# Optimization experiments

Measured on AMD Instinct MI355X. Metric: run time of the kernel, lower is better.

## Reference

```python
import jax, jax.numpy as jnp
import numpy as np

N = 262144          # num keyframes
E = 1048576         # num visual links (edges)
DT = 0.1            # IMU integration step
L1, L2, L3, L4 = 1.0, 0.5, 2.0, 0.5
EPS = 1e-6

# ---- quaternion helpers (pypose convention: q = [x, y, z, w]) ----

def qmul(q1, q2):
    v1, w1 = q1[..., :3], q1[..., 3:4]
    v2, w2 = q2[..., :3], q2[..., 3:4]
    w = w1 * w2 - jnp.sum(v1 * v2, axis=-1, keepdims=True)
    v = w1 * v2 + w2 * v1 + jnp.cross(v1, v2)
    return jnp.concatenate([v, w], axis=-1)

def qconj(q):
    return jnp.concatenate([-q[..., :3], q[..., 3:4]], axis=-1)

def qrot(q, x):
    # rotate vector x by unit quaternion q: x + 2*cross(v, cross(v,x) + w*x)
    v, w = q[..., :3], q[..., 3:4]
    return x + 2.0 * jnp.cross(v, jnp.cross(v, x) + w * x)

def so3_log(q):
    # log map of unit quaternion -> axis-angle phi (..., 3)
    v, w = q[..., :3], q[..., 3:4]
    n = jnp.linalg.norm(v, axis=-1, keepdims=True)
    n_safe = jnp.where(n < EPS, 1.0, n)
    theta = 2.0 * jnp.arctan2(n, w)
    w_safe = jnp.where(jnp.abs(w) < EPS, 1.0, w)
    factor = jnp.where(n < EPS, 2.0 / w_safe, theta / n_safe)
    return factor * v

def se3_inv(p):
    t, q = p[..., :3], p[..., 3:]
    qi = qconj(q)
    ti = -qrot(qi, t)
    return jnp.concatenate([ti, qi], axis=-1)

def se3_mul(p1, p2):
    t1, q1 = p1[..., :3], p1[..., 3:]
    t2, q2 = p2[..., :3], p2[..., 3:]
    t = t1 + qrot(q1, t2)
    return jnp.concatenate([t, qmul(q1, q2)], axis=-1)

def se3_log(p):
    # returns se(3) tensor [tau, phi] (pypose order) with tau = Jl^{-1}(phi) t
    t, q = p[..., :3], p[..., 3:]
    phi = so3_log(q)
    th = jnp.linalg.norm(phi, axis=-1, keepdims=True)
    th_safe = jnp.where(th < EPS, 1.0, th)
    coef = jnp.where(
        th < EPS,
        1.0 / 12.0 + th * th / 720.0,
        1.0 / (th_safe * th_safe)
        - (1.0 + jnp.cos(th_safe)) / (2.0 * th_safe * jnp.sin(th_safe)),
    )
    pxt = jnp.cross(phi, t)
    tau = t - 0.5 * pxt + coef * jnp.cross(phi, pxt)
    return jnp.concatenate([tau, phi], axis=-1)


def setup_inputs() -> dict:
    key = jax.random.key(0)
    ks = jax.random.split(key, 8)

    def unit_quat(k, n):
        q = jax.random.normal(k, (n, 4), dtype=jnp.float32)
        return q / jnp.linalg.norm(q, axis=-1, keepdims=True)

    pose = jnp.concatenate(
        [jax.random.normal(ks[0], (N, 3), dtype=jnp.float32),
         unit_quat(ks[1], N)], axis=-1)
    vel = jax.random.normal(ks[2], (N, 3), dtype=jnp.float32)
    vmot = jnp.concatenate(
        [0.1 * jax.random.normal(ks[3], (E, 3), dtype=jnp.float32),
         unit_quat(ks[4], E)], axis=-1)
    imu_drot = unit_quat(ks[5], N - 1)
    body_dvel = 0.1 * jax.random.normal(ks[6], (N - 1, 3), dtype=jnp.float32)
    body_dpos = 0.1 * jax.random.normal(ks[7], (N - 1, 3), dtype=jnp.float32)
    vlink = jax.random.randint(jax.random.fold_in(key, 99), (E, 2), 0, N)
    return dict(pose=pose, vel=vel, vmot=vmot, imu_drot=imu_drot,
                body_dvel=body_dvel, body_dpos=body_dpos, vlink=vlink)


def reference(pose, vel, vmot, imu_drot, body_dvel, body_dpos, vlink):
    trans, rot = pose[:, :3], pose[:, 3:]
    r1 = rot[:-1]

    # IMU model: world-frame increments (rotation-dependent, as in original)
    imu_dvel = qrot(r1, body_dvel)                      # world_dvel(pose.rotation())
    imu_dpos = qrot(r1, body_dpos) + vel[:-1] * DT      # world_dpos(rot, vel)

    # pose-graph residual: Log(vmot^{-1} @ pose1^{-1} @ pose2)  [E, 6]
    pose1 = pose[vlink[:, 0]]
    pose2 = pose[vlink[:, 1]]
    err = se3_mul(se3_inv(vmot), se3_mul(se3_inv(pose1), pose2))
    pgerr = se3_log(err)

    # adjacent velocity residual [N-1, 3]
    adjvelerr = imu_dvel - jnp.diff(vel, axis=0)

    # IMU rotation residual: Log(imu_drot @ R1^{-1} @ R2)  [N-1, 3]
    q_rel = qmul(imu_drot, qmul(qconj(rot[:-1]), rot[1:]))
    imuroterr = so3_log(q_rel)

    # translation/velocity residual [N-1, 3]
    transvelerr = imu_dpos - jnp.diff(trans, axis=0)

    return jnp.concatenate([
        L1 * pgerr.reshape(-1),
        L2 * adjvelerr.reshape(-1),
        L3 * imuroterr.reshape(-1),
        L4 * transvelerr.reshape(-1),
    ], axis=0)
```

## Files before the change

### kernel.cpp

```cpp
#include <hip/hip_runtime.h>
#include <math.h>

constexpr int   NN  = 262144;
constexpr int   NE  = 1048576;
constexpr float DTc = 0.1f;
constexpr float W1 = 1.0f, W2 = 0.5f, W3 = 2.0f, W4 = 0.5f;
constexpr float EPSc = 1e-6f;

typedef float    __attribute__((ext_vector_type(2))) f32x2;
typedef float    __attribute__((ext_vector_type(4))) f32x4;
typedef float    __attribute__((ext_vector_type(4), aligned(4))) f32x4u;
typedef float    __attribute__((ext_vector_type(2), aligned(4))) f32x2u;
typedef int      __attribute__((ext_vector_type(2))) i32x2;
typedef _Float16 __attribute__((ext_vector_type(8))) f16x8;

struct V3 { float x, y, z; };
struct Q4 { float x, y, z, w; };

__device__ __forceinline__ V3 v3(float x, float y, float z) { V3 r{x, y, z}; return r; }
__device__ __forceinline__ V3 vadd(V3 a, V3 b) { return v3(a.x + b.x, a.y + b.y, a.z + b.z); }
__device__ __forceinline__ V3 vsub(V3 a, V3 b) { return v3(a.x - b.x, a.y - b.y, a.z - b.z); }
__device__ __forceinline__ V3 vscale(float s, V3 a) { return v3(s * a.x, s * a.y, s * a.z); }
__device__ __forceinline__ V3 vcross(V3 a, V3 b) {
    return v3(a.y * b.z - a.z * b.y, a.z * b.x - a.x * b.z, a.x * b.y - a.y * b.x);
}
__device__ __forceinline__ float vdot(V3 a, V3 b) { return a.x * b.x + a.y * b.y + a.z * b.z; }

__device__ __forceinline__ Q4 qmul(Q4 a, Q4 b) {
    Q4 r;
    r.w = a.w * b.w - (a.x * b.x + a.y * b.y + a.z * b.z);
    r.x = a.w * b.x + b.w * a.x + (a.y * b.z - a.z * b.y);
    r.y = a.w * b.y + b.w * a.y + (a.z * b.x - a.x * b.z);
    r.z = a.w * b.z + b.w * a.z + (a.x * b.y - a.y * b.x);
    return r;
}
__device__ __forceinline__ Q4 qconj(Q4 q) { Q4 r{-q.x, -q.y, -q.z, q.w}; return r; }
__device__ __forceinline__ V3 qrot(Q4 q, V3 x) {
    V3 v = v3(q.x, q.y, q.z);
    V3 c1 = vadd(vcross(v, x), vscale(q.w, x));
    return vadd(x, vscale(2.0f, vcross(v, c1)));
}
__device__ __forceinline__ V3 so3_log(Q4 q) {
    V3 v = v3(q.x, q.y, q.z);
    float n = sqrtf(vdot(v, v));
    float theta = 2.0f * atan2f(n, q.w);
    float factor;
    if (n < EPSc) {
        float w_safe = (fabsf(q.w) < EPSc) ? 1.0f : q.w;
        factor = 2.0f / w_safe;
    } else {
        factor = theta / n;
    }
    return vscale(factor, v);
}

struct TP { V3 tau; V3 phi; };

__device__ __forceinline__ TP edge_residual(V3 tm, Q4 qm, V3 t1, Q4 q1,
                                            V3 t2, Q4 q2) {
    Q4 qa = qconj(q1);
    V3 tb = qrot(qa, vsub(t2, t1));
    Q4 qb = qmul(qa, q2);
    Q4 qc = qconj(qm);
    V3 te = qrot(qc, vsub(tb, tm));
    Q4 qe = qmul(qc, qb);

    V3 phi = so3_log(qe);
    float th = sqrtf(vdot(phi, phi));
    float coef;
    if (th < EPSc) {
        coef = 1.0f / 12.0f + th * th / 720.0f;
    } else {
        float s, c;
        sincosf(th, &s, &c);
        coef = 1.0f / (th * th) - (1.0f + c) / (2.0f * th * s);
    }
    V3 pxt = vcross(phi, te);
    V3 tau = vadd(vsub(te, vscale(0.5f, pxt)), vscale(coef, vcross(phi, pxt)));
    TP r; r.tau = tau; r.phi = phi; return r;
}

__global__ __launch_bounds__(256) void node_pack_kernel(
    const float* __restrict__ pose, const float* __restrict__ vel,
    const float* __restrict__ imu_drot, const float* __restrict__ body_dvel,
    const float* __restrict__ body_dpos, f16x8* __restrict__ ppH,
    float* __restrict__ out)
{
    int i = blockIdx.x * blockDim.x + threadIdx.x;
    if (i >= NN) return;
    f32x4u pa0 = *(const f32x4u*)(pose + 7 * (size_t)i);
    f32x4u pa1 = *(const f32x4u*)(pose + 7 * (size_t)i + 3);
    f16x8 rec = {(_Float16)pa0.x, (_Float16)pa0.y, (_Float16)pa0.z,
                 (_Float16)pa1.x, (_Float16)pa1.y, (_Float16)pa1.z,
                 (_Float16)pa1.w, (_Float16)0.0f};
    ppH[i] = rec;
    if (i >= NN - 1) return;

    V3 tr1 = v3(pa0.x, pa0.y, pa0.z); Q4 r1 = {pa1.x, pa1.y, pa1.z, pa1.w};
    f32x4u pb0 = *(const f32x4u*)(pose + 7 * (size_t)(i + 1));
    f32x4u pb1 = *(const f32x4u*)(pose + 7 * (size_t)(i + 1) + 3);
    V3 tr2 = v3(pb0.x, pb0.y, pb0.z); Q4 r2 = {pb1.x, pb1.y, pb1.z, pb1.w};

    f32x4u vv = __builtin_nontemporal_load((const f32x4u*)(vel + 3 * (size_t)i));
    f32x2u vw = __builtin_nontemporal_load((const f32x2u*)(vel + 3 * (size_t)i + 4));
    V3 v1 = v3(vv.x, vv.y, vv.z);
    V3 v2 = v3(vv.w, vw.x, vw.y);
    f32x2u bv0 = __builtin_nontemporal_load((const f32x2u*)(body_dvel + 3 * (size_t)i));
    float  bv2 = __builtin_nontemporal_load(body_dvel + 3 * (size_t)i + 2);
    f32x2u bp0 = __builtin_nontemporal_load((const f32x2u*)(body_dpos + 3 * (size_t)i));
    float  bp2 = __builtin_nontemporal_load(body_dpos + 3 * (size_t)i + 2);
    V3 bdv = v3(bv0.x, bv0.y, bv2);
    V3 bdp = v3(bp0.x, bp0.y, bp2);
    f32x4 id4 = __builtin_nontemporal_load((const f32x4*)(imu_drot + 4 * (size_t)i));
    Q4 idr = {id4.x, id4.y, id4.z, id4.w};

    V3 imu_dvel = qrot(r1, bdv);
    V3 adjvel = vsub(imu_dvel, vsub(v2, v1));
    Q4 qrel = qmul(idr, qmul(qconj(r1), r2));
    V3 imurot = so3_log(qrel);
    V3 imu_dpos = vadd(qrot(r1, bdp), vscale(DTc, v1));
    V3 transvel = vsub(imu_dpos, vsub(tr2, tr1));

    size_t base = (size_t)6 * NE;
    size_t nm1 = (size_t)(NN - 1);
    float* oa = out + base + 3 * (size_t)i;
    __builtin_nontemporal_store(W2 * adjvel.x, oa);
    __builtin_nontemporal_store(W2 * adjvel.y, oa + 1);
    __builtin_nontemporal_store(W2 * adjvel.z, oa + 2);
    float* ob = out + base + 3 * nm1 + 3 * (size_t)i;
    __builtin_nontemporal_store(W3 * imurot.x, ob);
    __builtin_nontemporal_store(W3 * imurot.y, ob + 1);
    __builtin_nontemporal_store(W3 * imurot.z, ob + 2);
    float* oc = out + base + 6 * nm1 + 3 * (size_t)i;
    __builtin_nontemporal_store(W4 * transvel.x, oc);
    __builtin_nontemporal_store(W4 * transvel.y, oc + 1);
    __builtin_nontemporal_store(W4 * transvel.z, oc + 2);
}

__global__ __launch_bounds__(256) void edge_kernel(
    const float* __restrict__ vmot, const int* __restrict__ vlink,
    const f16x8* __restrict__ ppH, float* __restrict__ out)
{
    __shared__ float smv[256 * 7];
    int e0 = blockIdx.x * 256;
    const f32x4* src = (const f32x4*)(vmot + (size_t)e0 * 7);
    {
        int idx = threadIdx.x;
        ((f32x4*)smv)[idx] = __builtin_nontemporal_load(src + idx);
        idx += 256;
        if (idx < 448) ((f32x4*)smv)[idx] = __builtin_nontemporal_load(src + idx);
    }
    int e = e0 + threadIdx.x;
    i32x2 l = __builtin_nontemporal_load((const i32x2*)vlink + e);
    f16x8 g1 = ppH[l.x];
    f16x8 g2 = ppH[l.y];
    __syncthreads();
    float m[7];
#pragma unroll
    for (int k = 0; k < 7; ++k) m[k] = smv[7 * threadIdx.x + k];

    TP r = edge_residual(
        v3(m[0], m[1], m[2]), Q4{m[3], m[4], m[5], m[6]},
        v3((float)g1[0], (float)g1[1], (float)g1[2]),
        Q4{(float)g1[3], (float)g1[4], (float)g1[5], (float)g1[6]},
        v3((float)g2[0], (float)g2[1], (float)g2[2]),
        Q4{(float)g2[3], (float)g2[4], (float)g2[5], (float)g2[6]});

    f32x2* o2 = (f32x2*)(out + 6 * (size_t)e);
    f32x2 a = {W1 * r.tau.x, W1 * r.tau.y};
    f32x2 b = {W1 * r.tau.z, W1 * r.phi.x};
    f32x2 c = {W1 * r.phi.y, W1 * r.phi.z};
    __builtin_nontemporal_store(a, o2);
    __builtin_nontemporal_store(b, o2 + 1);
    __builtin_nontemporal_store(c, o2 + 2);
}

__global__ __launch_bounds__(256) void vigraph_fallback(
    const float* __restrict__ pose, const float* __restrict__ vel,
    const float* __restrict__ vmot, const float* __restrict__ imu_drot,
    const float* __restrict__ body_dvel, const float* __restrict__ body_dpos,
    const int* __restrict__ vlink, float* __restrict__ out)
{
    int tid = blockIdx.x * blockDim.x + threadIdx.x;
    if (tid < NE) {
        int e = tid;
        const float* pm = vmot + 7 * (size_t)e;
        int i1 = vlink[2 * (size_t)e];
        int i2 = vlink[2 * (size_t)e + 1];
        const float* p1 = pose + 7 * (size_t)i1;
        const float* p2 = pose + 7 * (size_t)i2;
        TP r = edge_residual(v3(pm[0], pm[1], pm[2]), Q4{pm[3], pm[4], pm[5], pm[6]},
                             v3(p1[0], p1[1], p1[2]), Q4{p1[3], p1[4], p1[5], p1[6]},
                             v3(p2[0], p2[1], p2[2]), Q4{p2[3], p2[4], p2[5], p2[6]});
        float* o = out + 6 * (size_t)e;
        o[0] = W1 * r.tau.x; o[1] = W1 * r.tau.y; o[2] = W1 * r.tau.z;
        o[3] = W1 * r.phi.x; o[4] = W1 * r.phi.y; o[5] = W1 * r.phi.z;
    } else {
        int i = tid - NE;
        if (i >= NN - 1) return;
        const float* pa = pose + 7 * (size_t)i;
        const float* pb = pose + 7 * (size_t)(i + 1);
        V3 tr1 = v3(pa[0], pa[1], pa[2]); Q4 r1 = {pa[3], pa[4], pa[5], pa[6]};
        V3 tr2 = v3(pb[0], pb[1], pb[2]); Q4 r2 = {pb[3], pb[4], pb[5], pb[6]};
        V3 v1 = v3(vel[3 * (size_t)i], vel[3 * (size_t)i + 1], vel[3 * (size_t)i + 2]);
        V3 v2 = v3(vel[3 * (size_t)(i + 1)], vel[3 * (size_t)(i + 1) + 1], vel[3 * (size_t)(i + 1) + 2]);
        V3 bdv = v3(body_dvel[3 * (size_t)i], body_dvel[3 * (size_t)i + 1], body_dvel[3 * (size_t)i + 2]);
        V3 bdp = v3(body_dpos[3 * (size_t)i], body_dpos[3 * (size_t)i + 1], body_dpos[3 * (size_t)i + 2]);
        Q4 idr = {imu_drot[4 * (size_t)i], imu_drot[4 * (size_t)i + 1],
                  imu_drot[4 * (size_t)i + 2], imu_drot[4 * (size_t)i + 3]};
        V3 imu_dvel = qrot(r1, bdv);
        V3 adjvel = vsub(imu_dvel, vsub(v2, v1));
        Q4 qrel = qmul(idr, qmul(qconj(r1), r2));
        V3 imurot = so3_log(qrel);
        V3 imu_dpos = vadd(qrot(r1, bdp), vscale(DTc, v1));
        V3 transvel = vsub(imu_dpos, vsub(tr2, tr1));
        size_t base = (size_t)6 * NE;
        size_t nm1 = (size_t)(NN - 1);
        float* oa = out + base + 3 * (size_t)i;
        oa[0] = W2 * adjvel.x; oa[1] = W2 * adjvel.y; oa[2] = W2 * adjvel.z;
        float* ob = out + base + 3 * nm1 + 3 * (size_t)i;
        ob[0] = W3 * imurot.x; ob[1] = W3 * imurot.y; ob[2] = W3 * imurot.z;
        float* oc = out + base + 6 * nm1 + 3 * (size_t)i;
        oc[0] = W4 * transvel.x; oc[1] = W4 * transvel.y; oc[2] = W4 * transvel.z;
    }
}

extern "C" void kernel_launch(void* const* d_in, const int* in_sizes, int n_in,
                              void* d_out, int out_size, void* d_ws, size_t ws_size,
                              hipStream_t stream) {
    const float* pose      = (const float*)d_in[0];
    const float* vel       = (const float*)d_in[1];
    const float* vmot      = (const float*)d_in[2];
    const float* imu_drot  = (const float*)d_in[3];
    const float* body_dvel = (const float*)d_in[4];
    const float* body_dpos = (const float*)d_in[5];
    const int*   vlink     = (const int*)d_in[6];
    float* out = (float*)d_out;

    const size_t table_bytes = (size_t)NN * 16;
    if (ws_size >= table_bytes) {
        f16x8* ppH = (f16x8*)d_ws;
        node_pack_kernel<<<NN / 256, 256, 0, stream>>>(pose, vel, imu_drot,
                                                       body_dvel, body_dpos, ppH, out);
        edge_kernel<<<NE / 256, 256, 0, stream>>>(vmot, vlink, ppH, out);
    } else {
        int total = NE + (NN - 1);
        int grid = (total + 255) / 256;
        vigraph_fallback<<<grid, 256, 0, stream>>>(pose, vel, vmot, imu_drot,
                                                   body_dvel, body_dpos, vlink, out);
    }
}
```

Baseline: 39.71 us.

## Split pose packing from node residuals and interleave node work into edge kernel

The node kernel is reduced to a minimal fp16 pose-pack pass, and the IMU/node residual work moves into the edge kernel. Blocks are interleaved four edge blocks to one node block, so the bandwidth-heavy node residual work overlaps with the gather-bound edge work. The edge path also drops the shared-memory staging of vmot and its __syncthreads in favour of direct unaligned vector loads per thread. The trade-offs are uncoalesced per-thread vmot loads and a second read of pose in the fused kernel.

```diff
diff --git a/kernel.cpp b/kernel.cpp
--- a/kernel.cpp
+++ b/kernel.cpp
@@ -6,6 +6,10 @@
 constexpr float DTc = 0.1f;
 constexpr float W1 = 1.0f, W2 = 0.5f, W3 = 2.0f, W4 = 0.5f;
 constexpr float EPSc = 1e-6f;
+
+constexpr int NB_EDGE = NE / 256;
+constexpr int NB_NODE = NN / 256;
+constexpr int NB_TOT  = NB_EDGE + NB_NODE;
 
 typedef float    __attribute__((ext_vector_type(2))) f32x2;
 typedef float    __attribute__((ext_vector_type(4))) f32x4;
@@ -80,99 +84,96 @@
     TP r; r.tau = tau; r.phi = phi; return r;
 }
 
-__global__ __launch_bounds__(256) void node_pack_kernel(
+__global__ __launch_bounds__(256) void pack_kernel(const float* __restrict__ pose,
+                                                   f16x8* __restrict__ ppH) {
+    int i = blockIdx.x * blockDim.x + threadIdx.x;
+    if (i >= NN) return;
+    f32x4u a = *(const f32x4u*)(pose + 7 * (size_t)i);
+    f32x4u b = *(const f32x4u*)(pose + 7 * (size_t)i + 3);
+    f16x8 rec = {(_Float16)a.x, (_Float16)a.y, (_Float16)a.z,
+                 (_Float16)b.x, (_Float16)b.y, (_Float16)b.z,
+                 (_Float16)b.w, (_Float16)0.0f};
+    ppH[i] = rec;
+}
+
+__global__ __launch_bounds__(256) void fused_kernel(
     const float* __restrict__ pose, const float* __restrict__ vel,
-    const float* __restrict__ imu_drot, const float* __restrict__ body_dvel,
-    const float* __restrict__ body_dpos, f16x8* __restrict__ ppH,
+    const float* __restrict__ vmot, const float* __restrict__ imu_drot,
+    const float* __restrict__ body_dvel, const float* __restrict__ body_dpos,
+    const int* __restrict__ vlink, const f16x8* __restrict__ ppH,
     float* __restrict__ out)
 {
-    int i = blockIdx.x * blockDim.x + threadIdx.x;
-    if (i >= NN) return;
-    f32x4u pa0 = *(const f32x4u*)(pose + 7 * (size_t)i);
-    f32x4u pa1 = *(const f32x4u*)(pose + 7 * (size_t)i + 3);
-    f16x8 rec = {(_Float16)pa0.x, (_Float16)pa0.y, (_Float16)pa0.z,
-                 (_Float16)pa1.x, (_Float16)pa1.y, (_Float16)pa1.z,
-                 (_Float16)pa1.w, (_Float16)0.0f};
-    ppH[i] = rec;
-    if (i >= NN - 1) return;
-
-    V3 tr1 = v3(pa0.x, pa0.y, pa0.z); Q4 r1 = {pa1.x, pa1.y, pa1.z, pa1.w};
-    f32x4u pb0 = *(const f32x4u*)(pose + 7 * (size_t)(i + 1));
-    f32x4u pb1 = *(const f32x4u*)(pose + 7 * (size_t)(i + 1) + 3);
-    V3 tr2 = v3(pb0.x, pb0.y, pb0.z); Q4 r2 = {pb1.x, pb1.y, pb1.z, pb1.w};
-
-    f32x4u vv = __builtin_nontemporal_load((const f32x4u*)(vel + 3 * (size_t)i));
-    f32x2u vw = __builtin_nontemporal_load((const f32x2u*)(vel + 3 * (size_t)i + 4));
-    V3 v1 = v3(vv.x, vv.y, vv.z);
-    V3 v2 = v3(vv.w, vw.x, vw.y);
-    f32x2u bv0 = __builtin_nontemporal_load((const f32x2u*)(body_dvel + 3 * (size_t)i));
-    float  bv2 = __builtin_nontemporal_load(body_dvel + 3 * (size_t)i + 2);
-    f32x2u bp0 = __builtin_nontemporal_load((const f32x2u*)(body_dpos + 3 * (size_t)i));
-    float  bp2 = __builtin_nontemporal_load(body_dpos + 3 * (size_t)i + 2);
-    V3 bdv = v3(bv0.x, bv0.y, bv2);
-    V3 bdp = v3(bp0.x, bp0.y, bp2);
-    f32x4 id4 = __builtin_nontemporal_load((const f32x4*)(imu_drot + 4 * (size_t)i));
-    Q4 idr = {id4.x, id4.y, id4.z, id4.w};
-
-    V3 imu_dvel = qrot(r1, bdv);
-    V3 adjvel = vsub(imu_dvel, vsub(v2, v1));
-    Q4 qrel = qmul(idr, qmul(qconj(r1), r2));
-    V3 imurot = so3_log(qrel);
-    V3 imu_dpos = vadd(qrot(r1, bdp), vscale(DTc, v1));
-    V3 transvel = vsub(imu_dpos, vsub(tr2, tr1));
-
-    size_t base = (size_t)6 * NE;
-    size_t nm1 = (size_t)(NN - 1);
-    float* oa = out + base + 3 * (size_t)i;
-    __builtin_nontemporal_store(W2 * adjvel.x, oa);
-    __builtin_nontemporal_store(W2 * adjvel.y, oa + 1);
-    __builtin_nontemporal_store(W2 * adjvel.z, oa + 2);
-    float* ob = out + base + 3 * nm1 + 3 * (size_t)i;
-    __builtin_nontemporal_store(W3 * imurot.x, ob);
-    __builtin_nontemporal_store(W3 * imurot.y, ob + 1);
-    __builtin_nontemporal_store(W3 * imurot.z, ob + 2);
-    float* oc = out + base + 6 * nm1 + 3 * (size_t)i;
-    __builtin_nontemporal_store(W4 * transvel.x, oc);
-    __builtin_nontemporal_store(W4 * transvel.y, oc + 1);
-    __builtin_nontemporal_store(W4 * transvel.z, oc + 2);
-}
-
-__global__ __launch_bounds__(256) void edge_kernel(
-    const float* __restrict__ vmot, const int* __restrict__ vlink,
-    const f16x8* __restrict__ ppH, float* __restrict__ out)
-{
-    __shared__ float smv[256 * 7];
-    int e0 = blockIdx.x * 256;
-    const f32x4* src = (const f32x4*)(vmot + (size_t)e0 * 7);
-    {
-        int idx = threadIdx.x;
-        ((f32x4*)smv)[idx] = __builtin_nontemporal_load(src + idx);
-        idx += 256;
-        if (idx < 448) ((f32x4*)smv)[idx] = __builtin_nontemporal_load(src + idx);
-    }
-    int e = e0 + threadIdx.x;
-    i32x2 l = __builtin_nontemporal_load((const i32x2*)vlink + e);
-    f16x8 g1 = ppH[l.x];
-    f16x8 g2 = ppH[l.y];
-    __syncthreads();
-    float m[7];
-#pragma unroll
-    for (int k = 0; k < 7; ++k) m[k] = smv[7 * threadIdx.x + k];
-
-    TP r = edge_residual(
-        v3(m[0], m[1], m[2]), Q4{m[3], m[4], m[5], m[6]},
-        v3((float)g1[0], (float)g1[1], (float)g1[2]),
-        Q4{(float)g1[3], (float)g1[4], (float)g1[5], (float)g1[6]},
-        v3((float)g2[0], (float)g2[1], (float)g2[2]),
-        Q4{(float)g2[3], (float)g2[4], (float)g2[5], (float)g2[6]});
-
-    f32x2* o2 = (f32x2*)(out + 6 * (size_t)e);
-    f32x2 a = {W1 * r.tau.x, W1 * r.tau.y};
-    f32x2 b = {W1 * r.tau.z, W1 * r.phi.x};
-    f32x2 c = {W1 * r.phi.y, W1 * r.phi.z};
-    __builtin_nontemporal_store(a, o2);
-    __builtin_nontemporal_store(b, o2 + 1);
-    __builtin_nontemporal_store(c, o2 + 2);
+    int b = blockIdx.x;
+    int g = b / 5, rdx = b - 5 * g;
+    if (rdx < 4) {
+        int eb = g * 4 + rdx;
+        int e  = eb * 256 + threadIdx.x;
+        i32x2 l = __builtin_nontemporal_load((const i32x2*)vlink + e);
+        const float* pm = vmot + 7 * (size_t)e;
+        f32x4u ma = __builtin_nontemporal_load((const f32x4u*)(pm));
+        f32x4u mb = __builtin_nontemporal_load((const f32x4u*)(pm + 3));
+        f16x8 g1 = ppH[l.x];
+        f16x8 g2 = ppH[l.y];
+
+        TP r = edge_residual(
+            v3(ma.x, ma.y, ma.z), Q4{mb.x, mb.y, mb.z, mb.w},
+            v3((float)g1[0], (float)g1[1], (float)g1[2]),
+            Q4{(float)g1[3], (float)g1[4], (float)g1[5], (float)g1[6]},
+            v3((float)g2[0], (float)g2[1], (float)g2[2]),
+            Q4{(float)g2[3], (float)g2[4], (float)g2[5], (float)g2[6]});
+
+        f32x2* o2 = (f32x2*)(out + 6 * (size_t)e);
+        f32x2 a = {W1 * r.tau.x, W1 * r.tau.y};
+        f32x2 bb = {W1 * r.tau.z, W1 * r.phi.x};
+        f32x2 c = {W1 * r.phi.y, W1 * r.phi.z};
+        __builtin_nontemporal_store(a, o2);
+        __builtin_nontemporal_store(bb, o2 + 1);
+        __builtin_nontemporal_store(c, o2 + 2);
+    } else {
+        int i = g * 256 + threadIdx.x;
+        if (i >= NN - 1) return;
+        f32x4u pa0 = __builtin_nontemporal_load((const f32x4u*)(pose + 7 * (size_t)i));
+        f32x4u pa1 = __builtin_nontemporal_load((const f32x4u*)(pose + 7 * (size_t)i + 3));
+        V3 tr1 = v3(pa0.x, pa0.y, pa0.z); Q4 r1 = {pa1.x, pa1.y, pa1.z, pa1.w};
+        f32x4u pb0 = __builtin_nontemporal_load((const f32x4u*)(pose + 7 * (size_t)(i + 1)));
+        f32x4u pb1 = __builtin_nontemporal_load((const f32x4u*)(pose + 7 * (size_t)(i + 1) + 3));
+        V3 tr2 = v3(pb0.x, pb0.y, pb0.z); Q4 r2 = {pb1.x, pb1.y, pb1.z, pb1.w};
+
+        f32x4u vv = __builtin_nontemporal_load((const f32x4u*)(vel + 3 * (size_t)i));
+        f32x2u vw = __builtin_nontemporal_load((const f32x2u*)(vel + 3 * (size_t)i + 4));
+        V3 v1 = v3(vv.x, vv.y, vv.z);
+        V3 v2 = v3(vv.w, vw.x, vw.y);
+        f32x2u bv0 = __builtin_nontemporal_load((const f32x2u*)(body_dvel + 3 * (size_t)i));
+        float  bv2 = __builtin_nontemporal_load(body_dvel + 3 * (size_t)i + 2);
+        f32x2u bp0 = __builtin_nontemporal_load((const f32x2u*)(body_dpos + 3 * (size_t)i));
+        float  bp2 = __builtin_nontemporal_load(body_dpos + 3 * (size_t)i + 2);
+        V3 bdv = v3(bv0.x, bv0.y, bv2);
+        V3 bdp = v3(bp0.x, bp0.y, bp2);
+        f32x4 id4 = __builtin_nontemporal_load((const f32x4*)(imu_drot + 4 * (size_t)i));
+        Q4 idr = {id4.x, id4.y, id4.z, id4.w};
+
+        V3 imu_dvel = qrot(r1, bdv);
+        V3 adjvel = vsub(imu_dvel, vsub(v2, v1));
+        Q4 qrel = qmul(idr, qmul(qconj(r1), r2));
+        V3 imurot = so3_log(qrel);
+        V3 imu_dpos = vadd(qrot(r1, bdp), vscale(DTc, v1));
+        V3 transvel = vsub(imu_dpos, vsub(tr2, tr1));
+
+        size_t base = (size_t)6 * NE;
+        size_t nm1 = (size_t)(NN - 1);
+        float* oa = out + base + 3 * (size_t)i;
+        __builtin_nontemporal_store(W2 * adjvel.x, oa);
+        __builtin_nontemporal_store(W2 * adjvel.y, oa + 1);
+        __builtin_nontemporal_store(W2 * adjvel.z, oa + 2);
+        float* ob = out + base + 3 * nm1 + 3 * (size_t)i;
+        __builtin_nontemporal_store(W3 * imurot.x, ob);
+        __builtin_nontemporal_store(W3 * imurot.y, ob + 1);
+        __builtin_nontemporal_store(W3 * imurot.z, ob + 2);
+        float* oc = out + base + 6 * nm1 + 3 * (size_t)i;
+        __builtin_nontemporal_store(W4 * transvel.x, oc);
+        __builtin_nontemporal_store(W4 * transvel.y, oc + 1);
+        __builtin_nontemporal_store(W4 * transvel.z, oc + 2);
+    }
 }
 
 __global__ __launch_bounds__(256) void vigraph_fallback(
@@ -240,9 +241,9 @@
     const size_t table_bytes = (size_t)NN * 16;
     if (ws_size >= table_bytes) {
         f16x8* ppH = (f16x8*)d_ws;
-        node_pack_kernel<<<NN / 256, 256, 0, stream>>>(pose, vel, imu_drot,
-                                                       body_dvel, body_dpos, ppH, out);
-        edge_kernel<<<NE / 256, 256, 0, stream>>>(vmot, vlink, ppH, out);
+        pack_kernel<<<NB_NODE, 256, 0, stream>>>(pose, ppH);
+        fused_kernel<<<NB_TOT, 256, 0, stream>>>(pose, vel, vmot, imu_drot,
+                                                 body_dvel, body_dpos, vlink, ppH, out);
     } else {
         int total = NE + (NN - 1);
         int grid = (total + 255) / 256;
```

Measured after the change: 44.20 us. 11.3% more time.
